# Performance work log

Hardware: AMD Instinct MI355X
Metric: run time of the kernel (lower is better)

Reference implementation:

```python
import jax, jax.numpy as jnp
import numpy as np

D_MODEL = 1024
N_HEADS = 16
D_K = D_MODEL // N_HEADS
B, S = 2, 2048


def setup_inputs() -> dict:
    key = jax.random.key(0)
    ks = jax.random.split(key, 12)
    scale = 1.0 / np.sqrt(D_MODEL)
    inp = {
        "query": jax.random.normal(ks[0], (B, S, D_MODEL), jnp.float32),
        "key": jax.random.normal(ks[1], (B, S, D_MODEL), jnp.float32),
        "value": jax.random.normal(ks[2], (B, S, D_MODEL), jnp.float32),
        "mask": jnp.tril(jnp.ones((S, S), dtype=bool))[None, None],  # (1,1,S,S) causal
        "W_q": jax.random.normal(ks[3], (D_MODEL, D_MODEL), jnp.float32) * scale,
        "b_q": jnp.zeros((D_MODEL,), jnp.float32),
        "W_k": jax.random.normal(ks[4], (D_MODEL, D_MODEL), jnp.float32) * scale,
        "b_k": jnp.zeros((D_MODEL,), jnp.float32),
        "W_v": jax.random.normal(ks[5], (D_MODEL, D_MODEL), jnp.float32) * scale,
        "b_v": jnp.zeros((D_MODEL,), jnp.float32),
        "W_o": jax.random.normal(ks[6], (D_MODEL, D_MODEL), jnp.float32) * scale,
        "b_o": jnp.zeros((D_MODEL,), jnp.float32),
    }
    return inp


def reference(query, key, value, mask, W_q, b_q, W_k, b_k, W_v, b_v, W_o, b_o):
    b = query.shape[0]
    # Linear projections (torch Linear: x @ W.T + b), split into heads -> (b,h,s,d_k)
    def proj(x, W, bias):
        y = x @ W.T + bias
        return y.reshape(b, -1, N_HEADS, D_K).transpose(0, 2, 1, 3)

    q = proj(query, W_q, b_q)
    k = proj(key, W_k, b_k)
    v = proj(value, W_v, b_v)

    # scores: (b,h,sq,sk)
    scores = jnp.einsum("bhqd,bhkd->bhqk", q, k) / jnp.sqrt(jnp.float32(D_K)).astype(q.dtype)
    scores = jnp.where(mask, scores, jnp.finfo(scores.dtype).min)
    attn = jax.nn.softmax(scores, axis=-1)
    out = jnp.einsum("bhqk,bhkd->bhqd", attn, v)  # (b,h,sq,d_k)
    out = out.transpose(0, 2, 1, 3).reshape(b, -1, D_MODEL)
    return out @ W_o.T + b_o
```

## Files before the change

### kernel.cpp

```cpp
#include <hip/hip_runtime.h>
#include <hip/hip_bf16.h>
#include <stdint.h>

#define D_MODEL 1024
#define NH 16
#define DK 64
#define BB 2
#define SS 2048
#define MROWS (BB*SS)

typedef __attribute__((ext_vector_type(8))) short bf16x8;
typedef __attribute__((ext_vector_type(4))) float f32x4;

__device__ __forceinline__ short to_bf16(float f) {
  __hip_bfloat16 h = __float2bfloat16(f);
  union { __hip_bfloat16 b; short s; } u; u.b = h; return u.s;
}

__device__ __forceinline__ f32x4 mfma16(bf16x8 a, bf16x8 b, f32x4 c) {
  return __builtin_amdgcn_mfma_f32_16x16x32_bf16(a, b, c, 0, 0, 0);
}

__device__ __forceinline__ void gload_lds16(const void* g, void* l) {
  __builtin_amdgcn_global_load_lds(
      (const __attribute__((address_space(1))) unsigned int*)g,
      (__attribute__((address_space(3))) unsigned int*)l,
      16, 0, 0);
}

__device__ __forceinline__ float max3f(float a, float b, float c) {
  return fmaxf(fmaxf(a, b), c);
}

__global__ __launch_bounds__(256) void cvt7(const float* __restrict__ x0,
                                            const float* __restrict__ x1,
                                            const float* __restrict__ x2,
                                            const float* __restrict__ w0,
                                            const float* __restrict__ w1,
                                            const float* __restrict__ w2,
                                            const float* __restrict__ w3,
                                            short* __restrict__ y0,
                                            short* __restrict__ y1,
                                            short* __restrict__ y2,
                                            short* __restrict__ y3,
                                            short* __restrict__ y4,
                                            short* __restrict__ y5,
                                            short* __restrict__ y6) {
  const int z = blockIdx.z;
  const float* x; short* y; int n;
  switch (z) {
    case 0: x = x0; y = y0; n = MROWS * D_MODEL; break;
    case 1: x = x1; y = y1; n = MROWS * D_MODEL; break;
    case 2: x = x2; y = y2; n = MROWS * D_MODEL; break;
    case 3: x = w0; y = y3; n = D_MODEL * D_MODEL; break;
    case 4: x = w1; y = y4; n = D_MODEL * D_MODEL; break;
    case 5: x = w2; y = y5; n = D_MODEL * D_MODEL; break;
    default: x = w3; y = y6; n = D_MODEL * D_MODEL; break;
  }
  const int i = (blockIdx.x * 256 + threadIdx.x) * 4;
  if (i >= n) return;
  const float4 v = *(const float4*)(x + i);
  short4 o;
  o.x = to_bf16(v.x); o.y = to_bf16(v.y); o.z = to_bf16(v.z); o.w = to_bf16(v.w);
  *(short4*)(y + i) = o;
}

__global__ __launch_bounds__(256) void gemm_qkv(const short* __restrict__ Xq,
                                                const short* __restrict__ Xk,
                                                const short* __restrict__ Xv,
                                                const short* __restrict__ Wq,
                                                const short* __restrict__ Wk,
                                                const short* __restrict__ Wv,
                                                const float* __restrict__ bq,
                                                const float* __restrict__ bk,
                                                const float* __restrict__ bv,
                                                short* __restrict__ Qh,
                                                short* __restrict__ Kh,
                                                short* __restrict__ VT) {
  constexpr int K = 1024, NSTEP = K / 32;
  __shared__ __align__(16) char pool[49152];
  const int z = blockIdx.z;
  const short* A    = z == 0 ? Xq : z == 1 ? Xk : Xv;
  const short* Wt   = z == 0 ? Wq : z == 1 ? Wk : Wv;
  const float* bias = z == 0 ? bq : z == 1 ? bk : bv;

  const int tid = threadIdx.x;
  const int w = tid >> 6, lane = tid & 63;
  const int m0 = blockIdx.x * 128, n0 = blockIdx.y * 128;
  const int wm = w >> 1, wn = w & 1;
  const int fr = lane & 15, fg = lane >> 4;
  const int srow = tid >> 2;
  const int scolS = ((tid & 3) ^ ((srow >> 1) & 3)) * 8;
  const int scolD = (tid & 3) * 8;
  const int fcs = (fg ^ ((fr >> 1) & 3)) * 8;

  f32x4 acc[4][4] = {};

#define QKV_STAGE(buf, k0)                                                    \
  do {                                                                        \
    short* As_ = (short*)(pool + (buf) * 16384);                              \
    short* Bs_ = (short*)(pool + (buf) * 16384 + 8192);                       \
    _Pragma("unroll") for (int i = 0; i < 2; ++i) {                           \
      const int row = i * 64 + srow;                                          \
      gload_lds16(A  + (size_t)(m0 + row) * K + (k0) + scolS,                 \
                  As_ + row * 32 + scolD);                                    \
      gload_lds16(Wt + (size_t)(n0 + row) * K + (k0) + scolS,                 \
                  Bs_ + row * 32 + scolD);                                    \
    }                                                                         \
  } while (0)

  QKV_STAGE(0, 0);
  QKV_STAGE(1, 32);
  asm volatile("s_waitcnt vmcnt(4)" ::: "memory");
  __syncthreads();

  for (int t = 0; t < NSTEP; ++t) {
    if (t + 2 < NSTEP) QKV_STAGE((t + 2) % 3, (t + 2) * 32);

    const short* Ab = (const short*)(pool + (t % 3) * 16384);
    const short* Bb = (const short*)(pool + (t % 3) * 16384 + 8192);
    bf16x8 af[4], bfr[4];
#pragma unroll
    for (int i = 0; i < 4; ++i) {
      af[i]  = *(const bf16x8*)(Ab + (wm * 64 + i * 16 + fr) * 32 + fcs);
      bfr[i] = *(const bf16x8*)(Bb + (wn * 64 + i * 16 + fr) * 32 + fcs);
    }
    __builtin_amdgcn_s_setprio(1);
#pragma unroll
    for (int mi = 0; mi < 4; ++mi)
#pragma unroll
      for (int ni = 0; ni < 4; ++ni)
        acc[mi][ni] = mfma16(af[mi], bfr[ni], acc[mi][ni]);
    __builtin_amdgcn_s_setprio(0);

    if (t + 2 < NSTEP)
      asm volatile("s_waitcnt vmcnt(4)" ::: "memory");
    else
      asm volatile("s_waitcnt vmcnt(0)" ::: "memory");
    __syncthreads();
  }
#undef QKV_STAGE

  if (z < 2) {
    const float scale = (z == 0) ? 0.18033688011112042f : 1.0f;
    short* dst = (z == 0) ? Qh : Kh;
#pragma unroll
    for (int mi = 0; mi < 4; ++mi)
#pragma unroll
      for (int ni = 0; ni < 4; ++ni) {
        const int col = n0 + wn * 64 + ni * 16 + fr;
        const float bval = bias[col];
        const int h = col >> 6, d = col & 63;
#pragma unroll
        for (int r = 0; r < 4; ++r) {
          const int row = m0 + wm * 64 + mi * 16 + fg * 4 + r;
          const float val = (acc[mi][ni][r] + bval) * scale;
          const int b = row >> 11, s = row & (SS - 1);
          dst[((size_t)(b * NH + h) * SS + s) * DK + d] = to_bf16(val);
        }
      }
  } else {
    short* trs = (short*)pool;
#pragma unroll
    for (int mi = 0; mi < 4; ++mi)
#pragma unroll
      for (int ni = 0; ni < 4; ++ni) {
        const int dl = wn * 64 + ni * 16 + fr;
        const int s0 = wm * 64 + mi * 16 + fg * 4;
        const float bval = bias[n0 + dl];
        short4 sv = {to_bf16(acc[mi][ni][0] + bval), to_bf16(acc[mi][ni][1] + bval),
                     to_bf16(acc[mi][ni][2] + bval), to_bf16(acc[mi][ni][3] + bval)};
        *(short4*)(trs + dl * 128 + (s0 ^ ((dl & 7) << 3))) = sv;
      }
    __syncthreads();
    const int b = m0 >> 11, sbase = m0 & (SS - 1);
#pragma unroll
    for (int rep = 0; rep < 8; ++rep) {
      const int dl = (tid >> 4) + rep * 16;
      const int s0 = (tid & 15) * 8;
      const bf16x8 vv = *(const bf16x8*)(trs + dl * 128 + (s0 ^ ((dl & 7) << 3)));
      const int col = n0 + dl;
      const int h = col >> 6, d = col & 63;
      *(bf16x8*)(VT + ((size_t)(b * NH + h) * DK + d) * SS + sbase + s0) = vv;
    }
  }
}

__global__ __launch_bounds__(256) void gemm_out(const short* __restrict__ A,
                                                const short* __restrict__ Wt,
                                                const float* __restrict__ bias,
                                                float* __restrict__ Y) {
  constexpr int K = 1024, NSTEP = K / 32;
  __shared__ __align__(16) char pool[36864];
  const int tid = threadIdx.x;
  const int w = tid >> 6, lane = tid & 63;
  const int m0 = blockIdx.x * 128, n0 = blockIdx.y * 64;
  const int wm = w >> 1, wn = w & 1;
  const int fr = lane & 15, fg = lane >> 4;
  const int srow = tid >> 2;
  const int scolS = ((tid & 3) ^ ((srow >> 1) & 3)) * 8;
  const int scolD = (tid & 3) * 8;
  const int fcs = (fg ^ ((fr >> 1) & 3)) * 8;

  f32x4 acc[4][2] = {};

#define OUT_STAGE(buf, k0)                                                    \
  do {                                                                        \
    short* As_ = (short*)(pool + (buf) * 12288);                              \
    short* Bs_ = (short*)(pool + (buf) * 12288 + 8192);                       \
    _Pragma("unroll") for (int i = 0; i < 2; ++i) {                           \
      const int row = i * 64 + srow;                                          \
      gload_lds16(A + (size_t)(m0 + row) * K + (k0) + scolS,                  \
                  As_ + row * 32 + scolD);                                    \
    }                                                                         \
    gload_lds16(Wt + (size_t)(n0 + srow) * K + (k0) + scolS,                  \
                Bs_ + srow * 32 + scolD);                                     \
  } while (0)

  OUT_STAGE(0, 0);
  OUT_STAGE(1, 32);
  asm volatile("s_waitcnt vmcnt(3)" ::: "memory");
  __syncthreads();

  for (int t = 0; t < NSTEP; ++t) {
    if (t + 2 < NSTEP) OUT_STAGE((t + 2) % 3, (t + 2) * 32);

    const short* Ab = (const short*)(pool + (t % 3) * 12288);
    const short* Bb = (const short*)(pool + (t % 3) * 12288 + 8192);
    bf16x8 af[4], bfr[2];
#pragma unroll
    for (int i = 0; i < 4; ++i)
      af[i] = *(const bf16x8*)(Ab + (wm * 64 + i * 16 + fr) * 32 + fcs);
#pragma unroll
    for (int i = 0; i < 2; ++i)
      bfr[i] = *(const bf16x8*)(Bb + (wn * 32 + i * 16 + fr) * 32 + fcs);
    __builtin_amdgcn_s_setprio(1);
#pragma unroll
    for (int mi = 0; mi < 4; ++mi)
#pragma unroll
      for (int ni = 0; ni < 2; ++ni)
        acc[mi][ni] = mfma16(af[mi], bfr[ni], acc[mi][ni]);
    __builtin_amdgcn_s_setprio(0);

    if (t + 2 < NSTEP)
      asm volatile("s_waitcnt vmcnt(3)" ::: "memory");
    else
      asm volatile("s_waitcnt vmcnt(0)" ::: "memory");
    __syncthreads();
  }
#undef OUT_STAGE

#pragma unroll
  for (int mi = 0; mi < 4; ++mi)
#pragma unroll
    for (int ni = 0; ni < 2; ++ni) {
      const int col = n0 + wn * 32 + ni * 16 + fr;
      const float bval = bias[col];
#pragma unroll
      for (int r = 0; r < 4; ++r) {
        const int row = m0 + wm * 64 + mi * 16 + fg * 4 + r;
        Y[(size_t)row * D_MODEL + col] = acc[mi][ni][r] + bval;
      }
    }
}

__global__ __launch_bounds__(256) void attn_kernel(const short* __restrict__ Qh,
                                                   const short* __restrict__ Kh,
                                                   const short* __restrict__ VT,
                                                   short* __restrict__ AO) {
  __shared__ short Ks[2][2][64 * 64];
  __shared__ short Vs[2][2][64 * 64];
  __shared__ short P_lds[4][16 * 64];

  const int tid = threadIdx.x, w = tid >> 6, lane = tid & 63;
  const int fr = lane & 15, fg = lane >> 4;
  const int kr = fg * 4;
  const int swz = (fr & 7) << 4;

  const int bid = blockIdx.x;
  const int lid = ((bid & 7) << 6) | (bid >> 3);
  const int bh = lid >> 4;
  const int j = lid & 15;
  const int b = bh >> 4, h = bh & 15;

  const short* Qp = Qh + (size_t)bh * SS * DK;
  const short* Kp = Kh + (size_t)bh * SS * DK;
  const short* Vp = VT + (size_t)bh * DK * SS;

  const int sc_c = tid & 7;
  const int sc_r = tid >> 3;

  const int T0 = (j + 2) >> 1;
  const int koff0 = j * 64 - (T0 - 1) * 128;
  const int koff1 = (31 - j) * 64 - (16 - T0) * 128;

  bf16x8 qf[2];
#pragma unroll
  for (int hh = 0; hh < 2; ++hh)
    qf[hh] = *(const bf16x8*)(Qp + (size_t)(j * 64 + w * 16 + fr) * DK + hh * 32 + fg * 8);

  const short onev = (fr == 0) ? (short)0x3F80 : (short)0;
  const bf16x8 af4 = {onev, onev, onev, onev, onev, onev, onev, onev};

  f32x4 o[5] = {};
  float m_run = -1e30f;
  f32x4 stA[8], stB[8];

#define KK0(g) ((((g) < T0) ? (g) : ((g) - T0)) * 128)
#define STAGE_K(buf, kk0)                                                     \
  do {                                                                        \
    _Pragma("unroll") for (int hf = 0; hf < 2; ++hf)                          \
    _Pragma("unroll") for (int p = 0; p < 2; ++p) {                           \
      const int row = p * 32 + sc_r;                                          \
      const int sc = sc_c ^ (row & 7);                                        \
      gload_lds16(Kp + (size_t)((kk0) + hf * 64 + row) * DK + sc * 8,         \
                  &Ks[buf][hf][row * 64 + sc_c * 8]);                         \
    }                                                                         \
  } while (0)
#define STAGE_V(buf, kk0)                                                     \
  do {                                                                        \
    _Pragma("unroll") for (int hf = 0; hf < 2; ++hf)                          \
    _Pragma("unroll") for (int p = 0; p < 2; ++p) {                           \
      const int row = p * 32 + sc_r;                                          \
      const int sc = sc_c ^ (row & 7);                                        \
      gload_lds16(Vp + (size_t)row * SS + (kk0) + hf * 64 + sc * 8,           \
                  &Vs[buf][hf][row * 64 + sc_c * 8]);                         \
    }                                                                         \
  } while (0)

  auto softmax_pv = [&](int bufPrev) {
    float mm[8];
#pragma unroll
    for (int i = 0; i < 8; ++i)
      mm[i] = fmaxf(fmaxf(stB[i][0], stB[i][1]), fmaxf(stB[i][2], stB[i][3]));
    float pmax = fmaxf(max3f(mm[0], mm[1], mm[2]),
                       fmaxf(max3f(mm[3], mm[4], mm[5]), fmaxf(mm[6], mm[7])));
    pmax = fmaxf(pmax, __shfl_xor(pmax, 16));
    pmax = fmaxf(pmax, __shfl_xor(pmax, 32));

    if (!__all(pmax <= m_run + 11.0f)) {
      const float mn = fmaxf(m_run, pmax);
      const float al = __builtin_amdgcn_exp2f(m_run - mn);
      m_run = mn;
#pragma unroll
      for (int t = 0; t < 5; ++t)
#pragma unroll
        for (int r = 0; r < 4; ++r) o[t][r] *= al;
    }

#pragma unroll
    for (int hf = 0; hf < 2; ++hf) {
      char* base = (char*)P_lds[w];
#pragma unroll
      for (int kt = 0; kt < 4; ++kt) {
        short4 sv;
        sv.x = to_bf16(__builtin_amdgcn_exp2f(stB[hf * 4 + kt][0] - m_run));
        sv.y = to_bf16(__builtin_amdgcn_exp2f(stB[hf * 4 + kt][1] - m_run));
        sv.z = to_bf16(__builtin_amdgcn_exp2f(stB[hf * 4 + kt][2] - m_run));
        sv.w = to_bf16(__builtin_amdgcn_exp2f(stB[hf * 4 + kt][3] - m_run));
        *(short4*)(base + ((fr * 128 + kt * 32 + fg * 8) ^ swz)) = sv;
      }
      asm volatile("s_waitcnt lgkmcnt(0)" ::: "memory");

      const char* VsB = (const char*)Vs[bufPrev][hf];
      __builtin_amdgcn_s_setprio(1);
#pragma unroll
      for (int c = 0; c < 2; ++c) {
        const bf16x8 pf = *(const bf16x8*)((const char*)P_lds[w] +
                                           ((fr * 128 + c * 64 + fg * 16) ^ swz));
#pragma unroll
        for (int t = 0; t < 4; ++t) {
          const bf16x8 vfb = *(const bf16x8*)(VsB + (t * 16 + fr) * 128 +
                                              ((c * 64 + fg * 16) ^ swz));
          o[t] = mfma16(vfb, pf, o[t]);
        }
        o[4] = mfma16(af4, pf, o[4]);
      }
      __builtin_amdgcn_s_setprio(0);
    }
  };

  auto store_o = [&](int qbase) {
    const float l = __shfl(o[4][0], fr);
    const float inv = 1.0f / l;
    const int s = qbase + w * 16 + fr;
#pragma unroll
    for (int t = 0; t < 4; ++t) {
      short4 ov = {to_bf16(o[t][0] * inv), to_bf16(o[t][1] * inv),
                   to_bf16(o[t][2] * inv), to_bf16(o[t][3] * inv)};
      *(short4*)(AO + (size_t)(b * SS + s) * D_MODEL + h * 64 + t * 16 + kr) = ov;
    }
  };

  STAGE_K(0, 0);
  STAGE_V(0, 0);
  asm volatile("s_waitcnt vmcnt(0)" ::: "memory");
  __syncthreads();

  for (int g = 0; g < 17; ++g) {
    if (g == T0) {
#pragma unroll
      for (int hh = 0; hh < 2; ++hh)
        qf[hh] = *(const bf16x8*)(Qp + (size_t)((31 - j) * 64 + w * 16 + fr) * DK + hh * 32 + fg * 8);
    }

    if (g + 1 < 17) STAGE_K((g + 1) & 1, KK0(g + 1));

    {
      __builtin_amdgcn_s_setprio(1);
#pragma unroll
      for (int hf = 0; hf < 2; ++hf) {
        const char* KsB = (const char*)Ks[g & 1][hf];
#pragma unroll
        for (int kt = 0; kt < 4; ++kt) {
          const bf16x8 k0f = *(const bf16x8*)(KsB + (kt * 16 + fr) * 128 + ((fg * 16) ^ swz));
          const bf16x8 k1f = *(const bf16x8*)(KsB + (kt * 16 + fr) * 128 + ((64 + fg * 16) ^ swz));
          f32x4 zz = {};
          zz = mfma16(k0f, qf[0], zz);
          zz = mfma16(k1f, qf[1], zz);
          stA[hf * 4 + kt] = zz;
        }
      }
      __builtin_amdgcn_s_setprio(0);
    }
    if (g == T0 - 1 || g == 16) {
      const int koff = (g == 16) ? koff1 : koff0;
#pragma unroll
      for (int hf = 0; hf < 2; ++hf)
#pragma unroll
        for (int kt = 0; kt < 4; ++kt)
#pragma unroll
          for (int r = 0; r < 4; ++r)
            if (hf * 64 + kt * 16 + kr + r > koff + w * 16 + fr)
              stA[hf * 4 + kt][r] = -1e30f;
    }

    if (g > 0) {
      softmax_pv((g - 1) & 1);
      if (g == T0) {
        store_o(j * 64);
#pragma unroll
        for (int t = 0; t < 5; ++t)
#pragma unroll
          for (int r = 0; r < 4; ++r) o[t][r] = 0.f;
        m_run = -1e30f;
      }
    }

#pragma unroll
    for (int i = 0; i < 8; ++i) stB[i] = stA[i];

    __syncthreads();
    if (g + 1 < 17) {
      STAGE_V((g + 1) & 1, KK0(g + 1));
      asm volatile("s_waitcnt vmcnt(4)" ::: "memory");
    } else {
      asm volatile("s_waitcnt vmcnt(0)" ::: "memory");
    }
  }

  softmax_pv(16 & 1);
  store_o((31 - j) * 64);
#undef STAGE_K
#undef STAGE_V
#undef KK0
}

extern "C" void kernel_launch(void* const* d_in, const int* in_sizes, int n_in,
                              void* d_out, int out_size, void* d_ws, size_t ws_size,
                              hipStream_t stream) {
  const float* q  = (const float*)d_in[0];
  const float* k  = (const float*)d_in[1];
  const float* v  = (const float*)d_in[2];
  const float* Wq = (const float*)d_in[4];
  const float* bq = (const float*)d_in[5];
  const float* Wk = (const float*)d_in[6];
  const float* bk = (const float*)d_in[7];
  const float* Wv = (const float*)d_in[8];
  const float* bv = (const float*)d_in[9];
  const float* Wo = (const float*)d_in[10];
  const float* bo = (const float*)d_in[11];

  char* ws = (char*)d_ws;
  const size_t MB = 1u << 20;
  short* Xq = (short*)(ws + 0 * MB);
  short* Xk = (short*)(ws + 8 * MB);
  short* Xv = (short*)(ws + 16 * MB);
  short* Bq = (short*)(ws + 24 * MB);
  short* Bk = (short*)(ws + 26 * MB);
  short* Bv = (short*)(ws + 28 * MB);
  short* Bo = (short*)(ws + 30 * MB);
  short* Qh = (short*)(ws + 32 * MB);
  short* Kh = (short*)(ws + 40 * MB);
  short* VT = (short*)(ws + 48 * MB);
  short* AO = (short*)(ws + 56 * MB);

  cvt7<<<dim3(MROWS * D_MODEL / 1024, 1, 7), 256, 0, stream>>>(
      q, k, v, Wq, Wk, Wv, Wo, Xq, Xk, Xv, Bq, Bk, Bv, Bo);

  gemm_qkv<<<dim3(MROWS / 128, D_MODEL / 128, 3), 256, 0, stream>>>(
      Xq, Xk, Xv, Bq, Bk, Bv, bq, bk, bv, Qh, Kh, VT);

  attn_kernel<<<dim3(512), 256, 0, stream>>>(Qh, Kh, VT, AO);

  gemm_out<<<dim3(MROWS / 128, D_MODEL / 64), 256, 0, stream>>>(AO, Bo, bo, (float*)d_out);
}
```

Baseline: 118.7 us.

## Split paired causal attention blocks into one query tile per block

The attention kernel previously gave each block two 64-row query tiles (j and 31-j) for load balance, processing 128-key chunks over a fixed 17 steps. It now launches 1024 blocks, each handling a single 64-row query tile with 64-key chunks and a variable number of steps, ordered so heavy and light tiles interleave. The pipeline is unrolled two steps at a time with ping-pong score registers instead of copying stA to stB. This halves shared memory per block and raises occupancy and parallelism, but adds more barriers per key and loses the built-in balance of tile pairing.

After: 137.9 us. +16.2%, slower.

```diff
diff --git a/kernel.cpp b/kernel.cpp
--- a/kernel.cpp
+++ b/kernel.cpp
@@ -268,8 +268,8 @@
                                                    const short* __restrict__ Kh,
                                                    const short* __restrict__ VT,
                                                    short* __restrict__ AO) {
-  __shared__ short Ks[2][2][64 * 64];
-  __shared__ short Vs[2][2][64 * 64];
+  __shared__ short Ks[2][64 * 64];
+  __shared__ short Vs[2][64 * 64];
   __shared__ short P_lds[4][16 * 64];
 
   const int tid = threadIdx.x, w = tid >> 6, lane = tid & 63;
@@ -278,10 +278,13 @@
   const int swz = (fr & 7) << 4;
 
   const int bid = blockIdx.x;
-  const int lid = ((bid & 7) << 6) | (bid >> 3);
-  const int bh = lid >> 4;
-  const int j = lid & 15;
+  const int lid = ((bid & 7) << 7) | (bid >> 3);
+  const int bh = lid >> 5;
+  const int i5 = lid & 31;
+  const int j = (i5 & 1) ? (i5 >> 1) : (31 - (i5 >> 1));
   const int b = bh >> 4, h = bh & 15;
+  const int qb = j * 64;
+  const int T = j + 1;
 
   const short* Qp = Qh + (size_t)bh * SS * DK;
   const short* Kp = Kh + (size_t)bh * SS * DK;
@@ -290,180 +293,139 @@
   const int sc_c = tid & 7;
   const int sc_r = tid >> 3;
 
-  const int T0 = (j + 2) >> 1;
-  const int koff0 = j * 64 - (T0 - 1) * 128;
-  const int koff1 = (31 - j) * 64 - (16 - T0) * 128;
-
   bf16x8 qf[2];
 #pragma unroll
   for (int hh = 0; hh < 2; ++hh)
-    qf[hh] = *(const bf16x8*)(Qp + (size_t)(j * 64 + w * 16 + fr) * DK + hh * 32 + fg * 8);
+    qf[hh] = *(const bf16x8*)(Qp + (size_t)(qb + w * 16 + fr) * DK + hh * 32 + fg * 8);
 
   const short onev = (fr == 0) ? (short)0x3F80 : (short)0;
   const bf16x8 af4 = {onev, onev, onev, onev, onev, onev, onev, onev};
 
   f32x4 o[5] = {};
   float m_run = -1e30f;
-  f32x4 stA[8], stB[8];
-
-#define KK0(g) ((((g) < T0) ? (g) : ((g) - T0)) * 128)
+  f32x4 stA[4], stB[4];
+
 #define STAGE_K(buf, kk0)                                                     \
   do {                                                                        \
-    _Pragma("unroll") for (int hf = 0; hf < 2; ++hf)                          \
     _Pragma("unroll") for (int p = 0; p < 2; ++p) {                           \
       const int row = p * 32 + sc_r;                                          \
       const int sc = sc_c ^ (row & 7);                                        \
-      gload_lds16(Kp + (size_t)((kk0) + hf * 64 + row) * DK + sc * 8,         \
-                  &Ks[buf][hf][row * 64 + sc_c * 8]);                         \
+      gload_lds16(Kp + (size_t)((kk0) + row) * DK + sc * 8,                   \
+                  &Ks[buf][row * 64 + sc_c * 8]);                             \
     }                                                                         \
   } while (0)
 #define STAGE_V(buf, kk0)                                                     \
   do {                                                                        \
-    _Pragma("unroll") for (int hf = 0; hf < 2; ++hf)                          \
     _Pragma("unroll") for (int p = 0; p < 2; ++p) {                           \
       const int row = p * 32 + sc_r;                                          \
       const int sc = sc_c ^ (row & 7);                                        \
-      gload_lds16(Vp + (size_t)row * SS + (kk0) + hf * 64 + sc * 8,           \
-                  &Vs[buf][hf][row * 64 + sc_c * 8]);                         \
-    }                                                                         \
-  } while (0)
-
-  auto softmax_pv = [&](int bufPrev) {
-    float mm[8];
-#pragma unroll
-    for (int i = 0; i < 8; ++i)
-      mm[i] = fmaxf(fmaxf(stB[i][0], stB[i][1]), fmaxf(stB[i][2], stB[i][3]));
-    float pmax = fmaxf(max3f(mm[0], mm[1], mm[2]),
-                       fmaxf(max3f(mm[3], mm[4], mm[5]), fmaxf(mm[6], mm[7])));
-    pmax = fmaxf(pmax, __shfl_xor(pmax, 16));
-    pmax = fmaxf(pmax, __shfl_xor(pmax, 32));
-
-    if (!__all(pmax <= m_run + 11.0f)) {
-      const float mn = fmaxf(m_run, pmax);
-      const float al = __builtin_amdgcn_exp2f(m_run - mn);
-      m_run = mn;
-#pragma unroll
-      for (int t = 0; t < 5; ++t)
-#pragma unroll
-        for (int r = 0; r < 4; ++r) o[t][r] *= al;
-    }
-
-#pragma unroll
-    for (int hf = 0; hf < 2; ++hf) {
-      char* base = (char*)P_lds[w];
-#pragma unroll
-      for (int kt = 0; kt < 4; ++kt) {
-        short4 sv;
-        sv.x = to_bf16(__builtin_amdgcn_exp2f(stB[hf * 4 + kt][0] - m_run));
-        sv.y = to_bf16(__builtin_amdgcn_exp2f(stB[hf * 4 + kt][1] - m_run));
-        sv.z = to_bf16(__builtin_amdgcn_exp2f(stB[hf * 4 + kt][2] - m_run));
-        sv.w = to_bf16(__builtin_amdgcn_exp2f(stB[hf * 4 + kt][3] - m_run));
-        *(short4*)(base + ((fr * 128 + kt * 32 + fg * 8) ^ swz)) = sv;
-      }
-      asm volatile("s_waitcnt lgkmcnt(0)" ::: "memory");
-
-      const char* VsB = (const char*)Vs[bufPrev][hf];
-      __builtin_amdgcn_s_setprio(1);
-#pragma unroll
-      for (int c = 0; c < 2; ++c) {
-        const bf16x8 pf = *(const bf16x8*)((const char*)P_lds[w] +
-                                           ((fr * 128 + c * 64 + fg * 16) ^ swz));
-#pragma unroll
-        for (int t = 0; t < 4; ++t) {
-          const bf16x8 vfb = *(const bf16x8*)(VsB + (t * 16 + fr) * 128 +
-                                              ((c * 64 + fg * 16) ^ swz));
-          o[t] = mfma16(vfb, pf, o[t]);
-        }
-        o[4] = mfma16(af4, pf, o[4]);
-      }
-      __builtin_amdgcn_s_setprio(0);
-    }
-  };
-
-  auto store_o = [&](int qbase) {
-    const float l = __shfl(o[4][0], fr);
-    const float inv = 1.0f / l;
-    const int s = qbase + w * 16 + fr;
-#pragma unroll
-    for (int t = 0; t < 4; ++t) {
-      short4 ov = {to_bf16(o[t][0] * inv), to_bf16(o[t][1] * inv),
-                   to_bf16(o[t][2] * inv), to_bf16(o[t][3] * inv)};
-      *(short4*)(AO + (size_t)(b * SS + s) * D_MODEL + h * 64 + t * 16 + kr) = ov;
-    }
-  };
+      gload_lds16(Vp + (size_t)row * SS + (kk0) + sc * 8,                     \
+                  &Vs[buf][row * 64 + sc_c * 8]);                             \
+    }                                                                         \
+  } while (0)
+
+#define SOFTMAX_PV(ST, bufPrev)                                               \
+  do {                                                                        \
+    float mm0 = fmaxf(fmaxf(ST[0][0], ST[0][1]), fmaxf(ST[0][2], ST[0][3]));  \
+    float mm1 = fmaxf(fmaxf(ST[1][0], ST[1][1]), fmaxf(ST[1][2], ST[1][3]));  \
+    float mm2 = fmaxf(fmaxf(ST[2][0], ST[2][1]), fmaxf(ST[2][2], ST[2][3]));  \
+    float mm3 = fmaxf(fmaxf(ST[3][0], ST[3][1]), fmaxf(ST[3][2], ST[3][3]));  \
+    float pmax = fmaxf(fmaxf(mm0, mm1), fmaxf(mm2, mm3));                     \
+    pmax = fmaxf(pmax, __shfl_xor(pmax, 16));                                 \
+    pmax = fmaxf(pmax, __shfl_xor(pmax, 32));                                 \
+    if (!__all(pmax <= m_run + 11.0f)) {                                      \
+      const float mn = fmaxf(m_run, pmax);                                    \
+      const float al = __builtin_amdgcn_exp2f(m_run - mn);                    \
+      m_run = mn;                                                             \
+      _Pragma("unroll") for (int t = 0; t < 5; ++t)                           \
+        _Pragma("unroll") for (int r = 0; r < 4; ++r) o[t][r] *= al;          \
+    }                                                                         \
+    {                                                                         \
+      char* base = (char*)P_lds[w];                                           \
+      _Pragma("unroll") for (int kt = 0; kt < 4; ++kt) {                      \
+        short4 sv;                                                            \
+        sv.x = to_bf16(__builtin_amdgcn_exp2f(ST[kt][0] - m_run));            \
+        sv.y = to_bf16(__builtin_amdgcn_exp2f(ST[kt][1] - m_run));            \
+        sv.z = to_bf16(__builtin_amdgcn_exp2f(ST[kt][2] - m_run));            \
+        sv.w = to_bf16(__builtin_amdgcn_exp2f(ST[kt][3] - m_run));            \
+        *(short4*)(base + ((fr * 128 + kt * 32 + fg * 8) ^ swz)) = sv;        \
+      }                                                                       \
+    }                                                                         \
+    asm volatile("s_waitcnt lgkmcnt(0)" ::: "memory");                        \
+    {                                                                         \
+      const char* VsB = (const char*)Vs[bufPrev];                             \
+      __builtin_amdgcn_s_setprio(1);                                          \
+      _Pragma("unroll") for (int c = 0; c < 2; ++c) {                         \
+        const bf16x8 pf = *(const bf16x8*)((const char*)P_lds[w] +            \
+                                           ((fr * 128 + c * 64 + fg * 16) ^ swz)); \
+        _Pragma("unroll") for (int t = 0; t < 4; ++t) {                       \
+          const bf16x8 vfb = *(const bf16x8*)(VsB + (t * 16 + fr) * 128 +     \
+                                              ((c * 64 + fg * 16) ^ swz));    \
+          o[t] = mfma16(vfb, pf, o[t]);                                       \
+        }                                                                     \
+        o[4] = mfma16(af4, pf, o[4]);                                         \
+      }                                                                       \
+      __builtin_amdgcn_s_setprio(0);                                          \
+    }                                                                         \
+  } while (0)
+
+#define STEP(CUR, PREV, g)                                                    \
+  do {                                                                        \
+    if ((g) + 1 < T) STAGE_K(((g) + 1) & 1, ((g) + 1) * 64);                  \
+    {                                                                         \
+      const char* KsB = (const char*)Ks[(g) & 1];                             \
+      __builtin_amdgcn_s_setprio(1);                                          \
+      _Pragma("unroll") for (int kt = 0; kt < 4; ++kt) {                      \
+        const bf16x8 k0f = *(const bf16x8*)(KsB + (kt * 16 + fr) * 128 + ((fg * 16) ^ swz)); \
+        const bf16x8 k1f = *(const bf16x8*)(KsB + (kt * 16 + fr) * 128 + ((64 + fg * 16) ^ swz)); \
+        f32x4 zz = {};                                                        \
+        zz = mfma16(k0f, qf[0], zz);                                          \
+        zz = mfma16(k1f, qf[1], zz);                                          \
+        CUR[kt] = zz;                                                         \
+      }                                                                       \
+      __builtin_amdgcn_s_setprio(0);                                          \
+    }                                                                         \
+    if ((g) == T - 1) {                                                       \
+      _Pragma("unroll") for (int kt = 0; kt < 4; ++kt)                        \
+        _Pragma("unroll") for (int r = 0; r < 4; ++r)                         \
+          if (kt * 16 + kr + r > w * 16 + fr) CUR[kt][r] = -1e30f;            \
+    }                                                                         \
+    if ((g) > 0) SOFTMAX_PV(PREV, ((g) - 1) & 1);                             \
+    __syncthreads();                                                          \
+    if ((g) + 1 < T) {                                                        \
+      STAGE_V(((g) + 1) & 1, ((g) + 1) * 64);                                 \
+      asm volatile("s_waitcnt vmcnt(2)" ::: "memory");                        \
+    } else {                                                                  \
+      asm volatile("s_waitcnt vmcnt(0)" ::: "memory");                        \
+    }                                                                         \
+  } while (0)
 
   STAGE_K(0, 0);
   STAGE_V(0, 0);
-  asm volatile("s_waitcnt vmcnt(0)" ::: "memory");
+  asm volatile("s_waitcnt vmcnt(2)" ::: "memory");
   __syncthreads();
 
-  for (int g = 0; g < 17; ++g) {
-    if (g == T0) {
-#pragma unroll
-      for (int hh = 0; hh < 2; ++hh)
-        qf[hh] = *(const bf16x8*)(Qp + (size_t)((31 - j) * 64 + w * 16 + fr) * DK + hh * 32 + fg * 8);
-    }
-
-    if (g + 1 < 17) STAGE_K((g + 1) & 1, KK0(g + 1));
-
-    {
-      __builtin_amdgcn_s_setprio(1);
-#pragma unroll
-      for (int hf = 0; hf < 2; ++hf) {
-        const char* KsB = (const char*)Ks[g & 1][hf];
-#pragma unroll
-        for (int kt = 0; kt < 4; ++kt) {
-          const bf16x8 k0f = *(const bf16x8*)(KsB + (kt * 16 + fr) * 128 + ((fg * 16) ^ swz));
-          const bf16x8 k1f = *(const bf16x8*)(KsB + (kt * 16 + fr) * 128 + ((64 + fg * 16) ^ swz));
-          f32x4 zz = {};
-          zz = mfma16(k0f, qf[0], zz);
-          zz = mfma16(k1f, qf[1], zz);
-          stA[hf * 4 + kt] = zz;
-        }
-      }
-      __builtin_amdgcn_s_setprio(0);
-    }
-    if (g == T0 - 1 || g == 16) {
-      const int koff = (g == 16) ? koff1 : koff0;
-#pragma unroll
-      for (int hf = 0; hf < 2; ++hf)
-#pragma unroll
-        for (int kt = 0; kt < 4; ++kt)
-#pragma unroll
-          for (int r = 0; r < 4; ++r)
-            if (hf * 64 + kt * 16 + kr + r > koff + w * 16 + fr)
-              stA[hf * 4 + kt][r] = -1e30f;
-    }
-
-    if (g > 0) {
-      softmax_pv((g - 1) & 1);
-      if (g == T0) {
-        store_o(j * 64);
-#pragma unroll
-        for (int t = 0; t < 5; ++t)
-#pragma unroll
-          for (int r = 0; r < 4; ++r) o[t][r] = 0.f;
-        m_run = -1e30f;
-      }
-    }
-
-#pragma unroll
-    for (int i = 0; i < 8; ++i) stB[i] = stA[i];
-
-    __syncthreads();
-    if (g + 1 < 17) {
-      STAGE_V((g + 1) & 1, KK0(g + 1));
-      asm volatile("s_waitcnt vmcnt(4)" ::: "memory");
-    } else {
-      asm volatile("s_waitcnt vmcnt(0)" ::: "memory");
-    }
-  }
-
-  softmax_pv(16 & 1);
-  store_o((31 - j) * 64);
+  for (int gg = 0; gg < T; gg += 2) {
+    STEP(stA, stB, gg);
+    if (gg + 1 < T) STEP(stB, stA, gg + 1);
+  }
+
+  if (T & 1) SOFTMAX_PV(stA, (T - 1) & 1);
+  else       SOFTMAX_PV(stB, (T - 1) & 1);
+
+  const float l = __shfl(o[4][0], fr);
+  const float inv = 1.0f / l;
+  const int s = qb + w * 16 + fr;
+#pragma unroll
+  for (int t = 0; t < 4; ++t) {
+    short4 ov = {to_bf16(o[t][0] * inv), to_bf16(o[t][1] * inv),
+                 to_bf16(o[t][2] * inv), to_bf16(o[t][3] * inv)};
+    *(short4*)(AO + (size_t)(b * SS + s) * D_MODEL + h * 64 + t * 16 + kr) = ov;
+  }
+#undef STEP
+#undef SOFTMAX_PV
 #undef STAGE_K
 #undef STAGE_V
-#undef KK0
 }
 
 extern "C" void kernel_launch(void* const* d_in, const int* in_sizes, int n_in,
@@ -501,7 +463,7 @@
   gemm_qkv<<<dim3(MROWS / 128, D_MODEL / 128, 3), 256, 0, stream>>>(
       Xq, Xk, Xv, Bq, Bk, Bv, bq, bk, bv, Qh, Kh, VT);
 
-  attn_kernel<<<dim3(512), 256, 0, stream>>>(Qh, Kh, VT, AO);
+  attn_kernel<<<dim3(1024), 256, 0, stream>>>(Qh, Kh, VT, AO);
 
   gemm_out<<<dim3(MROWS / 128, D_MODEL / 64), 256, 0, stream>>>(AO, Bo, bo, (float*)d_out);
 }
```
